# Kernel optimization log

Hardware: AMD Instinct MI355X
Metric: run time of the kernel (lower is better)

## Reference

```python
import jax, jax.numpy as jnp
import numpy as np

IN_F, OUT_F, RANK = 4096, 4096, 1024
B, S = 4, 2048


def soft_threshold24(w):
    """Soft-threshold 2:4 sparsification along the last dim.
    For each group of 4, the two smallest-magnitude entries are zeroed and the
    kept entries are shrunk by the threshold (2nd-smallest magnitude)."""
    g = w.reshape(-1, 4)
    m = jnp.abs(g)
    t = jnp.sort(m, axis=-1)[:, 1:2]  # largest pruned magnitude per group
    sp = jnp.sign(g) * jnp.maximum(m - t, 0.0)
    return sp.reshape(w.shape)


def fake_fp8_mm(a, b):
    """FP8-simulated GEMM: fp16 operands, fp32 accumulate/output (matches fake_fp8_mm)."""
    return jnp.matmul(a.astype(jnp.float16), b.astype(jnp.float16),
                      preferred_element_type=jnp.float32)


def setup_inputs() -> dict:
    key = jax.random.key(0)
    k1, k2, k3 = jax.random.split(key, 3)
    x = jax.random.normal(k1, (B, S, IN_F), dtype=jnp.float32)
    std_a = (2.0 / (IN_F + RANK)) ** 0.5   # xavier_normal for (in_features, rank)
    std_b = (2.0 / (OUT_F + RANK)) ** 0.5  # xavier_normal for (out_features, rank)
    weight_A = jax.random.normal(k2, (IN_F, RANK), dtype=jnp.float32) * std_a
    weight_B = jax.random.normal(k3, (OUT_F, RANK), dtype=jnp.float32) * std_b
    bias = jnp.zeros((OUT_F,), dtype=jnp.float32)
    scale_A = jnp.ones((), dtype=jnp.float32)  # sparse_init_scale buffer
    scale_B = jnp.ones((), dtype=jnp.float32)
    return {"x": x, "weight_A": weight_A, "weight_B": weight_B, "bias": bias,
            "scale_A": scale_A, "scale_B": scale_B}


def reference(x, weight_A, weight_B, bias, scale_A, scale_B):
    # sparse low-rank factors
    wa = soft_threshold24(weight_A) * scale_A  # (in, rank)
    wb = soft_threshold24(weight_B) * scale_B  # (out, rank)
    lead = x.shape[:-1]
    xf = x.reshape(-1, x.shape[-1])            # (T, in)
    x_proj = fake_fp8_mm(xf, wa)               # (T, rank) == x @ A_sparse
    out = fake_fp8_mm(x_proj, wb.T) + bias     # (T, out) == x_proj @ B_sparse^T + b
    return out.reshape(*lead, OUT_F)
```

## Files before the change

### kernel.cpp

```cpp
#include <hip/hip_runtime.h>

#define IN_FEAT 4096
#define OUT_FEAT 4096
#define RANK 1024
#define TOK 8192

typedef _Float16 f16x8 __attribute__((ext_vector_type(8)));
typedef _Float16 f16x4 __attribute__((ext_vector_type(4)));
typedef float f32x4 __attribute__((ext_vector_type(4)));

#define GLD_LDS16(g, l)                                                         \
  __builtin_amdgcn_global_load_lds(                                             \
      (__attribute__((address_space(1))) const void*)(g),                       \
      (__attribute__((address_space(3))) void*)(l), 16, 0, 0)


__device__ __forceinline__ void soft24(const float4 g, float s,
                                       float& r0, float& r1, float& r2, float& r3) {
  const float m0 = fabsf(g.x), m1 = fabsf(g.y), m2 = fabsf(g.z), m3 = fabsf(g.w);
  const float lo1 = fminf(m0, m1), hi1 = fmaxf(m0, m1);
  const float lo2 = fminf(m2, m3), hi2 = fmaxf(m2, m3);
  const float t = fminf(fmaxf(lo1, lo2), fminf(hi1, hi2));
  r0 = copysignf(fmaxf(m0 - t, 0.0f), g.x) * s;
  r1 = copysignf(fmaxf(m1 - t, 0.0f), g.y) * s;
  r2 = copysignf(fmaxf(m2 - t, 0.0f), g.z) * s;
  r3 = copysignf(fmaxf(m3 - t, 0.0f), g.w) * s;
}

__global__ __launch_bounds__(256) void sparsify_A_kernel(
    const float* __restrict__ wA, const float* __restrict__ scaleA,
    _Float16* __restrict__ waT) {
  const int idx = blockIdx.x * 256 + threadIdx.x;
  const int i = idx & (IN_FEAT - 1);
  const int jg = idx >> 12;
  const float4 g = *reinterpret_cast<const float4*>(wA + (size_t)i * RANK + jg * 4);
  const float s = scaleA[0];
  float r0, r1, r2, r3;
  soft24(g, s, r0, r1, r2, r3);
  const size_t base = (size_t)(jg * 4) * IN_FEAT + i;
  waT[base] = (_Float16)r0;
  waT[base + IN_FEAT] = (_Float16)r1;
  waT[base + 2 * IN_FEAT] = (_Float16)r2;
  waT[base + 3 * IN_FEAT] = (_Float16)r3;
}

__global__ __launch_bounds__(256) void sparsify_B_kernel(
    const float* __restrict__ wB, const float* __restrict__ scaleB,
    _Float16* __restrict__ wbs) {
  const int idx = blockIdx.x * 256 + threadIdx.x;
  const float4 g = *reinterpret_cast<const float4*>(wB + (size_t)idx * 4);
  const float s = scaleB[0];
  float r0, r1, r2, r3;
  soft24(g, s, r0, r1, r2, r3);
  f16x4 h;
  h[0] = (_Float16)r0; h[1] = (_Float16)r1; h[2] = (_Float16)r2; h[3] = (_Float16)r3;
  *reinterpret_cast<f16x4*>(wbs + (size_t)idx * 4) = h;
}

__global__ __launch_bounds__(256) void cast_x_kernel(
    const float* __restrict__ x, _Float16* __restrict__ x16) {
  const size_t i = ((size_t)blockIdx.x * 256 + threadIdx.x) * 8;
  const float4 f0 = *reinterpret_cast<const float4*>(x + i);
  const float4 f1 = *reinterpret_cast<const float4*>(x + i + 4);
  f16x8 h;
  h[0] = (_Float16)f0.x; h[1] = (_Float16)f0.y;
  h[2] = (_Float16)f0.z; h[3] = (_Float16)f0.w;
  h[4] = (_Float16)f1.x; h[5] = (_Float16)f1.y;
  h[6] = (_Float16)f1.z; h[7] = (_Float16)f1.w;
  *reinterpret_cast<f16x8*>(x16 + i) = h;
}

template <int N, int K, bool A_F32, bool OUT_F16>
__global__ __launch_bounds__(256, 4) void gemm128(
    const void* __restrict__ Av, const _Float16* __restrict__ Bh,
    void* __restrict__ Cv, const float* __restrict__ bias) {
  __shared__ __attribute__((aligned(128))) char lds[32768];
  char* ldsA = lds;
  char* ldsB = lds + 16384;

  const int tid = threadIdx.x;
  const int lane = tid & 63;
  const int w = tid >> 6;
  const int wrow = (w >> 1) * 64;
  const int wcol = (w & 1) * 64;

  constexpr int GX = N / 128;
  const int nwg = GX * (TOK / 128);
  const int l = blockIdx.y * GX + blockIdx.x;
  const int wg = (l & 7) * (nwg >> 3) + (l >> 3);
  const int brow = (wg / GX) * 128;
  const int bcol = (wg % GX) * 128;

  f32x4 acc[4][4] = {};

  for (int k0 = 0; k0 < K; k0 += 64) {
    __syncthreads();
#pragma unroll
    for (int it = 0; it < 4; ++it) {
      const int c = it * 256 + tid;
      const int row = c >> 3;
      const int u = c & 7;
      const _Float16* gsrc =
          Bh + (size_t)(bcol + row) * K + k0 + ((u ^ (row & 7)) << 3);
      GLD_LDS16(gsrc, ldsB + c * 16);
    }
    if constexpr (A_F32) {
      const float* Af = (const float*)Av;
#pragma unroll
      for (int it = 0; it < 4; ++it) {
        const int c = it * 256 + tid;
        const int row = c >> 3;
        const int u = c & 7;
        const float* gsrc = Af + (size_t)(brow + row) * K + k0 + (u << 3);
        const float4 f0 = *reinterpret_cast<const float4*>(gsrc);
        const float4 f1 = *reinterpret_cast<const float4*>(gsrc + 4);
        f16x8 h;
        h[0] = (_Float16)f0.x; h[1] = (_Float16)f0.y;
        h[2] = (_Float16)f0.z; h[3] = (_Float16)f0.w;
        h[4] = (_Float16)f1.x; h[5] = (_Float16)f1.y;
        h[6] = (_Float16)f1.z; h[7] = (_Float16)f1.w;
        *reinterpret_cast<f16x8*>(ldsA + row * 128 + ((u ^ (row & 7)) << 4)) = h;
      }
    } else {
      const _Float16* Ah = (const _Float16*)Av;
#pragma unroll
      for (int it = 0; it < 4; ++it) {
        const int c = it * 256 + tid;
        const int row = c >> 3;
        const int u = c & 7;
        const _Float16* gsrc =
            Ah + (size_t)(brow + row) * K + k0 + ((u ^ (row & 7)) << 3);
        GLD_LDS16(gsrc, ldsA + c * 16);
      }
    }
    __syncthreads();
#pragma unroll
    for (int kk = 0; kk < 2; ++kk) {
      f16x8 af[4], bf[4];
#pragma unroll
      for (int m = 0; m < 4; ++m) {
        const int row = wrow + m * 16 + (lane & 15);
        const int u = (kk * 4 + (lane >> 4)) ^ (row & 7);
        af[m] = *reinterpret_cast<const f16x8*>(ldsA + row * 128 + u * 16);
      }
#pragma unroll
      for (int n = 0; n < 4; ++n) {
        const int row = wcol + n * 16 + (lane & 15);
        const int u = (kk * 4 + (lane >> 4)) ^ (row & 7);
        bf[n] = *reinterpret_cast<const f16x8*>(ldsB + row * 128 + u * 16);
      }
#pragma unroll
      for (int m = 0; m < 4; ++m)
#pragma unroll
        for (int n = 0; n < 4; ++n)
          acc[m][n] =
              __builtin_amdgcn_mfma_f32_16x16x32_f16(af[m], bf[n], acc[m][n], 0, 0, 0);
    }
  }

  const int r4 = (lane >> 4) * 4;
  const int cl = lane & 15;
  if constexpr (OUT_F16) {
    _Float16* C = (_Float16*)Cv;
#pragma unroll
    for (int m = 0; m < 4; ++m)
#pragma unroll
      for (int n = 0; n < 4; ++n)
#pragma unroll
        for (int j = 0; j < 4; ++j) {
          const int rr = brow + wrow + m * 16 + r4 + j;
          const int cc = bcol + wcol + n * 16 + cl;
          C[(size_t)rr * N + cc] = (_Float16)acc[m][n][j];
        }
  } else {
    float* C = (float*)Cv;
#pragma unroll
    for (int n = 0; n < 4; ++n) {
      const int cc = bcol + wcol + n * 16 + cl;
      const float bv = bias[cc];
#pragma unroll
      for (int m = 0; m < 4; ++m)
#pragma unroll
        for (int j = 0; j < 4; ++j) {
          const int rr = brow + wrow + m * 16 + r4 + j;
          C[(size_t)rr * N + cc] = acc[m][n][j] + bv;
        }
    }
  }
}

#define AOFF(s, h) (((s) * 2 + (h)) * 16384)
#define BOFF(s, h) (65536 + ((s) * 2 + (h)) * 16384)

#define MIDBAR()                                        \
  __builtin_amdgcn_s_barrier();                         \
  asm volatile("s_waitcnt lgkmcnt(0)" ::: "memory")
#define ENDBAR() __builtin_amdgcn_s_barrier()

#define QUAD(AF, BF, MO, NO)                                                   \
  __builtin_amdgcn_s_setprio(1);                                               \
  _Pragma("unroll") for (int ks = 0; ks < 2; ++ks)                             \
  _Pragma("unroll") for (int i = 0; i < 4; ++i)                                \
  _Pragma("unroll") for (int j = 0; j < 2; ++j)                                \
      acc[(MO) + i][(NO) + j] = __builtin_amdgcn_mfma_f32_16x16x32_f16(        \
          AF[i][ks], BF[j][ks], acc[(MO) + i][(NO) + j], 0, 0, 0);             \
  __builtin_amdgcn_s_setprio(0);

template <int M, int N, int K>
__global__ __launch_bounds__(512, 2) void gemm256(
    const _Float16* __restrict__ A, const _Float16* __restrict__ B,
    float* __restrict__ C, const float* __restrict__ bias) {
  extern __shared__ char lds[];

  const int tid = threadIdx.x;
  const int lane = tid & 63;
  const int w = tid >> 6;
  const int wr = w >> 2;
  const int wc = w & 3;
  const int l15 = lane & 15;
  const int ubase = lane >> 4;

  constexpr int GX = N / 256;
  constexpr int NWG = GX * (M / 256);
  const int l = blockIdx.y * GX + blockIdx.x;
  const int wg = (l & 7) * (NWG >> 3) + (l >> 3);
  const int brow = (wg / GX) * 256;
  const int bcol = (wg % GX) * 256;

  const _Float16* Abase = A + (size_t)brow * K;
  const _Float16* Bbase = B + (size_t)bcol * K;

  auto stage = [&](const _Float16* srcBase, int rowOff, int kof, int ldsOff) {
#pragma unroll
    for (int r = 0; r < 2; ++r) {
      const int c = r * 512 + tid;
      const int row = c >> 3;
      const int u = c & 7;
      const _Float16* g =
          srcBase + (size_t)(rowOff + row) * K + kof + ((u ^ (row & 7)) << 3);
      GLD_LDS16(g, lds + ldsOff + c * 16);
    }
  };

  f32x4 acc[8][4] = {};
  f16x8 af[4][2], bf01[2][2], bf23[2][2];

#define LDA_GRP(SLOT, MBASE)                                                   \
  _Pragma("unroll") for (int i = 0; i < 4; ++i)                                \
  _Pragma("unroll") for (int ks = 0; ks < 2; ++ks) {                           \
    const int row = ((MBASE) + i) * 16 + l15;                                  \
    const int u = (ks * 4 + ubase) ^ (row & 7);                                \
    af[i][ks] = *reinterpret_cast<const f16x8*>(                               \
        lds + AOFF(SLOT, wr) + row * 128 + u * 16);                            \
  }
#define LDB_GRP(SLOT, NBASE, DST)                                              \
  _Pragma("unroll") for (int j = 0; j < 2; ++j)                                \
  _Pragma("unroll") for (int ks = 0; ks < 2; ++ks) {                           \
    const int row = (wc & 1) * 64 + ((NBASE) + j) * 16 + l15;                  \
    const int u = (ks * 4 + ubase) ^ (row & 7);                                \
    DST[j][ks] = *reinterpret_cast<const f16x8*>(                              \
        lds + BOFF(SLOT, wc >> 1) + row * 128 + u * 16);                       \
  }

  constexpr int NT = K / 64;

  stage(Abase, 0, 0, AOFF(0, 0));
  stage(Abase, 128, 0, AOFF(0, 1));
  stage(Bbase, 0, 0, BOFF(0, 0));
  stage(Bbase, 128, 0, BOFF(0, 1));
  stage(Bbase, 0, 64, BOFF(1, 0));
  stage(Bbase, 128, 64, BOFF(1, 1));
  asm volatile("s_waitcnt vmcnt(4)" ::: "memory");
  __builtin_amdgcn_s_barrier();

  for (int tt = 0; tt < NT; tt += 2) {
    const bool last = (tt + 2 >= NT);
    const int kof1 = tt * 64 + 64;
    const int kof2 = tt * 64 + 128;
    const int kof3 = tt * 64 + 192;

    LDA_GRP(0, 0);
    LDB_GRP(0, 0, bf01);
    stage(Abase, 0, kof1, AOFF(1, 0));
    MIDBAR();
    QUAD(af, bf01, 0, 0);
    ENDBAR();
    LDB_GRP(0, 2, bf23);
    stage(Abase, 128, kof1, AOFF(1, 1));
    MIDBAR();
    QUAD(af, bf23, 0, 2);
    ENDBAR();
    LDA_GRP(0, 4);
    if (!last) stage(Bbase, 0, kof2, BOFF(0, 0));
    MIDBAR();
    QUAD(af, bf01, 4, 0);
    ENDBAR();
    if (!last) {
      stage(Bbase, 128, kof2, BOFF(0, 1));
      asm volatile("s_waitcnt vmcnt(4)" ::: "memory");
    } else {
      asm volatile("s_waitcnt vmcnt(0)" ::: "memory");
    }
    MIDBAR();
    QUAD(af, bf23, 4, 2);
    ENDBAR();
    LDA_GRP(1, 0);
    LDB_GRP(1, 0, bf01);
    if (!last) stage(Abase, 0, kof2, AOFF(0, 0));
    MIDBAR();
    QUAD(af, bf01, 0, 0);
    ENDBAR();
    LDB_GRP(1, 2, bf23);
    if (!last) stage(Abase, 128, kof2, AOFF(0, 1));
    MIDBAR();
    QUAD(af, bf23, 0, 2);
    ENDBAR();
    LDA_GRP(1, 4);
    if (!last) stage(Bbase, 0, kof3, BOFF(1, 0));
    MIDBAR();
    QUAD(af, bf01, 4, 0);
    ENDBAR();
    if (!last) {
      stage(Bbase, 128, kof3, BOFF(1, 1));
      asm volatile("s_waitcnt vmcnt(4)" ::: "memory");
    }
    MIDBAR();
    QUAD(af, bf23, 4, 2);
    ENDBAR();
  }

  const int r4 = (lane >> 4) * 4;
#pragma unroll
  for (int n = 0; n < 4; ++n) {
    const int cc = bcol + wc * 64 + n * 16 + l15;
    const float bv = bias[cc];
#pragma unroll
    for (int m = 0; m < 8; ++m)
#pragma unroll
      for (int j = 0; j < 4; ++j) {
        const int rr = brow + wr * 128 + m * 16 + r4 + j;
        C[(size_t)rr * N + cc] = acc[m][n][j] + bv;
      }
  }
}


extern "C" void kernel_launch(void* const* d_in, const int* in_sizes, int n_in,
                              void* d_out, int out_size, void* d_ws, size_t ws_size,
                              hipStream_t stream) {
  const float* x = (const float*)d_in[0];
  const float* wA = (const float*)d_in[1];
  const float* wB = (const float*)d_in[2];
  const float* bias = (const float*)d_in[3];
  const float* scaleA = (const float*)d_in[4];
  const float* scaleB = (const float*)d_in[5];
  float* out = (float*)d_out;

  char* ws = (char*)d_ws;
  _Float16* waT = (_Float16*)ws;
  _Float16* wbs = (_Float16*)(ws + (size_t)RANK * IN_FEAT * 2);
  _Float16* xp =
      (_Float16*)(ws + (size_t)RANK * IN_FEAT * 2 + (size_t)OUT_FEAT * RANK * 2);
  _Float16* x16 = (_Float16*)(ws + (size_t)RANK * IN_FEAT * 2 +
                              (size_t)OUT_FEAT * RANK * 2 + (size_t)TOK * RANK * 2);
  const size_t needed = (size_t)RANK * IN_FEAT * 2 + (size_t)OUT_FEAT * RANK * 2 +
                        (size_t)TOK * RANK * 2 + (size_t)TOK * IN_FEAT * 2;

  hipLaunchKernelGGL(sparsify_A_kernel, dim3((IN_FEAT * RANK / 4) / 256), dim3(256),
                     0, stream, wA, scaleA, waT);
  hipLaunchKernelGGL(sparsify_B_kernel, dim3((OUT_FEAT * RANK / 4) / 256), dim3(256),
                     0, stream, wB, scaleB, wbs);

  if (ws_size >= needed) {
    hipLaunchKernelGGL(cast_x_kernel, dim3((TOK * IN_FEAT / 8) / 256), dim3(256),
                       0, stream, x, x16);
    hipLaunchKernelGGL((gemm128<RANK, IN_FEAT, false, true>),
                       dim3(RANK / 128, TOK / 128), dim3(256), 0, stream,
                       (const void*)x16, waT, (void*)xp, nullptr);
  } else {
    hipLaunchKernelGGL((gemm128<RANK, IN_FEAT, true, true>),
                       dim3(RANK / 128, TOK / 128), dim3(256), 0, stream,
                       (const void*)x, waT, (void*)xp, nullptr);
  }

  (void)hipFuncSetAttribute(
      reinterpret_cast<const void*>(&gemm256<TOK, OUT_FEAT, RANK>),
      hipFuncAttributeMaxDynamicSharedMemorySize, 131072);
  hipLaunchKernelGGL((gemm256<TOK, OUT_FEAT, RANK>),
                     dim3(OUT_FEAT / 256, TOK / 256), dim3(512), 131072, stream,
                     xp, wbs, out, bias);
}
```

Before: 206.2 us.

## Add pipelined 128x256 tile kernel for first GEMM with LDS staging

Replaces the 128x128 256-thread GEMM used for x@A with a new 512-thread kernel using 128x256 tiles, XOR-swizzled LDS, direct global-to-LDS loads, double buffering with interleaved barriers, and XCD-aware workgroup remapping. It mirrors the schedule of the second GEMM kernel to overlap loads with MFMA and raise per-block reuse. It uses 96KB of dynamic LDS and requires K and tile divisibility. Only the cast-x path is changed.

Result: no change. 204.5 us (-0.8%).

```diff
diff --git a/kernel.cpp b/kernel.cpp
--- a/kernel.cpp
+++ b/kernel.cpp
@@ -13,6 +13,11 @@
   __builtin_amdgcn_global_load_lds(                                             \
       (__attribute__((address_space(1))) const void*)(g),                       \
       (__attribute__((address_space(3))) void*)(l), 16, 0, 0)
+
+#define MIDBAR()                                        \
+  __builtin_amdgcn_s_barrier();                         \
+  asm volatile("s_waitcnt lgkmcnt(0)" ::: "memory")
+#define ENDBAR() __builtin_amdgcn_s_barrier()
 
 
 __device__ __forceinline__ void soft24(const float4 g, float s,
@@ -189,13 +194,144 @@
   }
 }
 
+template <int M, int N, int K>
+__global__ __launch_bounds__(512, 2) void gemm1_k(
+    const _Float16* __restrict__ A, const _Float16* __restrict__ B,
+    _Float16* __restrict__ C) {
+  extern __shared__ char lds[];
+
+  const int tid = threadIdx.x;
+  const int lane = tid & 63;
+  const int w = tid >> 6;
+  const int wr = w >> 2;
+  const int wc = w & 3;
+  const int l15 = lane & 15;
+  const int ubase = lane >> 4;
+
+  constexpr int GX = N / 256;
+  constexpr int NWG = GX * (M / 128);
+  const int l = blockIdx.y * GX + blockIdx.x;
+  const int wg = (l & 7) * (NWG >> 3) + (l >> 3);
+  const int brow = (wg / GX) * 128;
+  const int bcol = (wg % GX) * 256;
+
+  f32x4 acc[4][4] = {};
+  f16x8 af[4][2], bf01[2][2], bf23[2][2];
+
+  auto lda = [&](int slot) {
+#pragma unroll
+    for (int i = 0; i < 4; ++i)
+#pragma unroll
+      for (int ks = 0; ks < 2; ++ks) {
+        const int row = wr * 64 + i * 16 + l15;
+        const int u = (ks * 4 + ubase) ^ (row & 7);
+        af[i][ks] =
+            *reinterpret_cast<const f16x8*>(lds + slot * 16384 + row * 128 + u * 16);
+      }
+  };
+  auto ldb = [&](int slot, int nbase, f16x8 (*dst)[2]) {
+#pragma unroll
+    for (int j = 0; j < 2; ++j)
+#pragma unroll
+      for (int ks = 0; ks < 2; ++ks) {
+        const int row = wc * 64 + (nbase + j) * 16 + l15;
+        const int u = (ks * 4 + ubase) ^ (row & 7);
+        dst[j][ks] = *reinterpret_cast<const f16x8*>(lds + 32768 + slot * 32768 +
+                                                     row * 128 + u * 16);
+      }
+  };
+  auto stageA = [&](int kof, int slot) {
+#pragma unroll
+    for (int r = 0; r < 2; ++r) {
+      const int c = r * 512 + tid;
+      const int row = c >> 3;
+      const int u = c & 7;
+      GLD_LDS16(A + (size_t)(brow + row) * K + kof + ((u ^ (row & 7)) << 3),
+                lds + slot * 16384 + c * 16);
+    }
+  };
+  auto stageB = [&](int kof, int slot) {
+#pragma unroll
+    for (int r = 0; r < 4; ++r) {
+      const int c = r * 512 + tid;
+      const int row = c >> 3;
+      const int u = c & 7;
+      GLD_LDS16(B + (size_t)(bcol + row) * K + kof + ((u ^ (row & 7)) << 3),
+                lds + 32768 + slot * 32768 + c * 16);
+    }
+  };
+
+#define QUAD16(BF, NO)                                                         \
+  __builtin_amdgcn_s_setprio(1);                                               \
+  _Pragma("unroll") for (int ks = 0; ks < 2; ++ks)                             \
+  _Pragma("unroll") for (int i = 0; i < 4; ++i)                                \
+  _Pragma("unroll") for (int j = 0; j < 2; ++j)                                \
+      acc[i][(NO) + j] = __builtin_amdgcn_mfma_f32_16x16x32_f16(               \
+          af[i][ks], BF[j][ks], acc[i][(NO) + j], 0, 0, 0);                    \
+  __builtin_amdgcn_s_setprio(0);
+
+  constexpr int NT = K / 64;
+
+  stageA(0, 0);
+  stageB(0, 0);
+  stageA(64, 1);
+  asm volatile("s_waitcnt vmcnt(2)" ::: "memory");
+  __builtin_amdgcn_s_barrier();
+
+  for (int tt = 0; tt < NT; tt += 2) {
+    const bool lastI = (tt + 2 >= NT);
+    const int kB1 = tt * 64 + 64;
+    const int kAB2 = tt * 64 + 128;
+    const int kA3 = tt * 64 + 192;
+
+    lda(0);
+    ldb(0, 0, bf01);
+    stageB(kB1, 1);
+    MIDBAR();
+    QUAD16(bf01, 0);
+    ENDBAR();
+    ldb(0, 2, bf23);
+    if (!lastI) {
+      stageA(kAB2, 0);
+      asm volatile("s_waitcnt vmcnt(2)" ::: "memory");
+    } else {
+      asm volatile("s_waitcnt vmcnt(0)" ::: "memory");
+    }
+    MIDBAR();
+    QUAD16(bf23, 2);
+    ENDBAR();
+    lda(1);
+    ldb(1, 0, bf01);
+    if (!lastI) stageB(kAB2, 0);
+    MIDBAR();
+    QUAD16(bf01, 0);
+    ENDBAR();
+    ldb(1, 2, bf23);
+    if (!lastI) {
+      stageA(kA3, 1);
+      asm volatile("s_waitcnt vmcnt(2)" ::: "memory");
+    }
+    MIDBAR();
+    QUAD16(bf23, 2);
+    ENDBAR();
+  }
+
+  const int r4 = (lane >> 4) * 4;
+#pragma unroll
+  for (int m = 0; m < 4; ++m)
+#pragma unroll
+    for (int n = 0; n < 4; ++n)
+#pragma unroll
+      for (int j = 0; j < 4; ++j) {
+        const int rr = brow + wr * 64 + m * 16 + r4 + j;
+        const int cc = bcol + wc * 64 + n * 16 + l15;
+        C[(size_t)rr * N + cc] = (_Float16)acc[m][n][j];
+      }
+#undef QUAD16
+}
+
 #define AOFF(s, h) (((s) * 2 + (h)) * 16384)
 #define BOFF(s, h) (65536 + ((s) * 2 + (h)) * 16384)
-
-#define MIDBAR()                                        \
-  __builtin_amdgcn_s_barrier();                         \
-  asm volatile("s_waitcnt lgkmcnt(0)" ::: "memory")
-#define ENDBAR() __builtin_amdgcn_s_barrier()
 
 #define QUAD(AF, BF, MO, NO)                                                   \
   __builtin_amdgcn_s_setprio(1);                                               \
@@ -285,16 +421,19 @@
     MIDBAR();
     QUAD(af, bf01, 0, 0);
     ENDBAR();
+
     LDB_GRP(0, 2, bf23);
     stage(Abase, 128, kof1, AOFF(1, 1));
     MIDBAR();
     QUAD(af, bf23, 0, 2);
     ENDBAR();
+
     LDA_GRP(0, 4);
     if (!last) stage(Bbase, 0, kof2, BOFF(0, 0));
     MIDBAR();
     QUAD(af, bf01, 4, 0);
     ENDBAR();
+
     if (!last) {
       stage(Bbase, 128, kof2, BOFF(0, 1));
       asm volatile("s_waitcnt vmcnt(4)" ::: "memory");
@@ -304,22 +443,26 @@
     MIDBAR();
     QUAD(af, bf23, 4, 2);
     ENDBAR();
+
     LDA_GRP(1, 0);
     LDB_GRP(1, 0, bf01);
     if (!last) stage(Abase, 0, kof2, AOFF(0, 0));
     MIDBAR();
     QUAD(af, bf01, 0, 0);
     ENDBAR();
+
     LDB_GRP(1, 2, bf23);
     if (!last) stage(Abase, 128, kof2, AOFF(0, 1));
     MIDBAR();
     QUAD(af, bf23, 0, 2);
     ENDBAR();
+
     LDA_GRP(1, 4);
     if (!last) stage(Bbase, 0, kof3, BOFF(1, 0));
     MIDBAR();
     QUAD(af, bf01, 4, 0);
     ENDBAR();
+
     if (!last) {
       stage(Bbase, 128, kof3, BOFF(1, 1));
       asm volatile("s_waitcnt vmcnt(4)" ::: "memory");
@@ -374,9 +517,12 @@
   if (ws_size >= needed) {
     hipLaunchKernelGGL(cast_x_kernel, dim3((TOK * IN_FEAT / 8) / 256), dim3(256),
                        0, stream, x, x16);
-    hipLaunchKernelGGL((gemm128<RANK, IN_FEAT, false, true>),
-                       dim3(RANK / 128, TOK / 128), dim3(256), 0, stream,
-                       (const void*)x16, waT, (void*)xp, nullptr);
+    (void)hipFuncSetAttribute(
+        reinterpret_cast<const void*>(&gemm1_k<TOK, RANK, IN_FEAT>),
+        hipFuncAttributeMaxDynamicSharedMemorySize, 98304);
+    hipLaunchKernelGGL((gemm1_k<TOK, RANK, IN_FEAT>),
+                       dim3(RANK / 256, TOK / 128), dim3(512), 98304, stream,
+                       x16, waT, xp);
   } else {
     hipLaunchKernelGGL((gemm128<RANK, IN_FEAT, true, true>),
                        dim3(RANK / 128, TOK / 128), dim3(256), 0, stream,
```
